# Kernel tuning notes

Hardware: AMD Instinct MI355X
Metric: run time of the kernel (lower is better)

Reference implementation:

```python
import jax, jax.numpy as jnp
import numpy as np

EPSILON = 1e-6
UP = 4
MAX_DEPTH = 10.0


def setup_inputs() -> dict:
    key = jax.random.key(0)
    k1, k2 = jax.random.split(key)
    feat = jax.random.normal(k1, (16, 4, 192, 192), dtype=jnp.float32)
    W = jax.random.normal(k2, (4, 4), dtype=jnp.float32)  # 1x1 conv weight [out,in]
    return {"feat": feat, "W": W}


def reference(feat, W):
    up = UP
    # 1x1 conv, no bias: [B,4,H,W] -> [B,4,H,W]
    plane_eq = jnp.einsum('oi,bihw->bohw', W, feat)
    # repeat_interleave upsample on H then W
    pe = jnp.repeat(jnp.repeat(plane_eq, up, axis=2), up, axis=3)
    p, q, r, s = pe[:, 0], pe[:, 1], pe[:, 2], pe[:, 3]  # [B, H*up, W*up]
    Hh, Ww = p.shape[1], p.shape[2]
    dt = feat.dtype
    base = jnp.arange(up, dtype=dt)
    # u cycles along width, v cycles along height, normalized pixel offsets
    u = (jnp.tile(base, Ww // up) - (up - 1) * 0.5) / up  # [Ww]
    v = (jnp.tile(base, Hh // up) - (up - 1) * 0.5) / up  # [Hh]
    norm = jnp.sqrt(p * p + q * q + r * r + EPSILON)
    pn = p / norm
    qn = q / norm
    rn = r / norm
    sn = s * norm
    disp = (pn * u[None, None, :] + qn * v[None, :, None] + rn) * sn
    disp = jnp.maximum(disp, 1.0 / MAX_DEPTH)[:, None]  # [B,1,Hh,Ww]
    return 1.0 / disp
```

## Files before the change

### kernel.cpp

```cpp
#include <hip/hip_runtime.h>
#include <hip/hip_bf16.h>


#define IN_H 192
#define IN_W 192
#define NBATCH 16
#define UPF 4
#define OUT_H (IN_H * UPF)
#define OUT_W (IN_W * UPF)

__global__ __launch_bounds__(256) void plane2depth_kernel(
    const float* __restrict__ feat,
    const float* __restrict__ Wm,
    float* __restrict__ out)
{
    const int npix = IN_H * IN_W;
    int idx = blockIdx.x * blockDim.x + threadIdx.x;
    if (idx >= NBATCH * npix) return;

    int b  = idx / npix;
    int hw = idx - b * npix;
    int h  = hw / IN_W;
    int w  = hw - h * IN_W;

    const float* f = feat + (size_t)b * 4 * npix + hw;
    float f0 = f[0];
    float f1 = f[npix];
    float f2 = f[2 * npix];
    float f3 = f[3 * npix];

    float p = Wm[0]  * f0 + Wm[1]  * f1 + Wm[2]  * f2 + Wm[3]  * f3;
    float q = Wm[4]  * f0 + Wm[5]  * f1 + Wm[6]  * f2 + Wm[7]  * f3;
    float r = Wm[8]  * f0 + Wm[9]  * f1 + Wm[10] * f2 + Wm[11] * f3;
    float s = Wm[12] * f0 + Wm[13] * f1 + Wm[14] * f2 + Wm[15] * f3;

    const float uv0 = -0.375f, uv1 = -0.125f, uv2 = 0.125f, uv3 = 0.375f;
    float pu0 = p * uv0, pu1 = p * uv1, pu2 = p * uv2, pu3 = p * uv3;

    float* o = out + (size_t)b * OUT_H * OUT_W + (size_t)(UPF * h) * OUT_W + UPF * w;

    const float vrow[4] = {uv0, uv1, uv2, uv3};
#pragma unroll
    for (int i = 0; i < 4; ++i) {
        float base = q * vrow[i] + r;
        float d0 = (pu0 + base) * s;
        float d1 = (pu1 + base) * s;
        float d2 = (pu2 + base) * s;
        float d3 = (pu3 + base) * s;
        float4 v4;
        v4.x = 1.0f / fmaxf(d0, 0.1f);
        v4.y = 1.0f / fmaxf(d1, 0.1f);
        v4.z = 1.0f / fmaxf(d2, 0.1f);
        v4.w = 1.0f / fmaxf(d3, 0.1f);
        *reinterpret_cast<float4*>(o + (size_t)i * OUT_W) = v4;
    }
}

extern "C" void kernel_launch(void* const* d_in, const int* in_sizes, int n_in,
                              void* d_out, int out_size, void* d_ws, size_t ws_size,
                              hipStream_t stream) {
    const float* feat = (const float*)d_in[0];
    const float* Wm   = (const float*)d_in[1];
    float* out        = (float*)d_out;

    const int total = NBATCH * IN_H * IN_W;
    const int block = 256;
    const int grid  = (total + block - 1) / block;
    plane2depth_kernel<<<grid, block, 0, stream>>>(feat, Wm, out);
}
```

Baseline: 73.04 us.

## Process two input pixels per thread with nontemporal stores and fast reciprocal

```diff
diff --git a/kernel.cpp b/kernel.cpp
--- a/kernel.cpp
+++ b/kernel.cpp
@@ -8,51 +8,67 @@
 #define UPF 4
 #define OUT_H (IN_H * UPF)
 #define OUT_W (IN_W * UPF)
+#define NPIX (IN_H * IN_W)
+#define NPAIR (NPIX / 2)
+
+typedef float f32x4 __attribute__((ext_vector_type(4)));
+typedef float f32x2 __attribute__((ext_vector_type(2)));
 
 __global__ __launch_bounds__(256) void plane2depth_kernel(
     const float* __restrict__ feat,
     const float* __restrict__ Wm,
     float* __restrict__ out)
 {
-    const int npix = IN_H * IN_W;
-    int idx = blockIdx.x * blockDim.x + threadIdx.x;
-    if (idx >= NBATCH * npix) return;
-
-    int b  = idx / npix;
-    int hw = idx - b * npix;
+    int t = blockIdx.x * blockDim.x + threadIdx.x;
+    int b  = t / NPAIR;
+    int pr = t - b * NPAIR;
+    int hw = pr * 2;
     int h  = hw / IN_W;
     int w  = hw - h * IN_W;
 
-    const float* f = feat + (size_t)b * 4 * npix + hw;
-    float f0 = f[0];
-    float f1 = f[npix];
-    float f2 = f[2 * npix];
-    float f3 = f[3 * npix];
+    const float* f = feat + (size_t)b * 4 * NPIX + hw;
+    f32x2 c0 = *reinterpret_cast<const f32x2*>(f);
+    f32x2 c1 = *reinterpret_cast<const f32x2*>(f + NPIX);
+    f32x2 c2 = *reinterpret_cast<const f32x2*>(f + 2 * NPIX);
+    f32x2 c3 = *reinterpret_cast<const f32x2*>(f + 3 * NPIX);
 
-    float p = Wm[0]  * f0 + Wm[1]  * f1 + Wm[2]  * f2 + Wm[3]  * f3;
-    float q = Wm[4]  * f0 + Wm[5]  * f1 + Wm[6]  * f2 + Wm[7]  * f3;
-    float r = Wm[8]  * f0 + Wm[9]  * f1 + Wm[10] * f2 + Wm[11] * f3;
-    float s = Wm[12] * f0 + Wm[13] * f1 + Wm[14] * f2 + Wm[15] * f3;
+    float w00 = Wm[0],  w01 = Wm[1],  w02 = Wm[2],  w03 = Wm[3];
+    float w10 = Wm[4],  w11 = Wm[5],  w12 = Wm[6],  w13 = Wm[7];
+    float w20 = Wm[8],  w21 = Wm[9],  w22 = Wm[10], w23 = Wm[11];
+    float w30 = Wm[12], w31 = Wm[13], w32 = Wm[14], w33 = Wm[15];
 
-    const float uv0 = -0.375f, uv1 = -0.125f, uv2 = 0.125f, uv3 = 0.375f;
-    float pu0 = p * uv0, pu1 = p * uv1, pu2 = p * uv2, pu3 = p * uv3;
+    float p0 = w00*c0.x + w01*c1.x + w02*c2.x + w03*c3.x;
+    float q0 = w10*c0.x + w11*c1.x + w12*c2.x + w13*c3.x;
+    float r0 = w20*c0.x + w21*c1.x + w22*c2.x + w23*c3.x;
+    float s0 = w30*c0.x + w31*c1.x + w32*c2.x + w33*c3.x;
+    float p1 = w00*c0.y + w01*c1.y + w02*c2.y + w03*c3.y;
+    float q1 = w10*c0.y + w11*c1.y + w12*c2.y + w13*c3.y;
+    float r1 = w20*c0.y + w21*c1.y + w22*c2.y + w23*c3.y;
+    float s1 = w30*c0.y + w31*c1.y + w32*c2.y + w33*c3.y;
+
+    const float uv[4] = {-0.375f, -0.125f, 0.125f, 0.375f};
+    float pu0[4], pu1[4];
+#pragma unroll
+    for (int j = 0; j < 4; ++j) { pu0[j] = p0 * uv[j]; pu1[j] = p1 * uv[j]; }
 
     float* o = out + (size_t)b * OUT_H * OUT_W + (size_t)(UPF * h) * OUT_W + UPF * w;
 
-    const float vrow[4] = {uv0, uv1, uv2, uv3};
 #pragma unroll
     for (int i = 0; i < 4; ++i) {
-        float base = q * vrow[i] + r;
-        float d0 = (pu0 + base) * s;
-        float d1 = (pu1 + base) * s;
-        float d2 = (pu2 + base) * s;
-        float d3 = (pu3 + base) * s;
-        float4 v4;
-        v4.x = 1.0f / fmaxf(d0, 0.1f);
-        v4.y = 1.0f / fmaxf(d1, 0.1f);
-        v4.z = 1.0f / fmaxf(d2, 0.1f);
-        v4.w = 1.0f / fmaxf(d3, 0.1f);
-        *reinterpret_cast<float4*>(o + (size_t)i * OUT_W) = v4;
+        float base0 = q0 * uv[i] + r0;
+        float base1 = q1 * uv[i] + r1;
+        f32x4 a, bb;
+        a.x  = __builtin_amdgcn_rcpf(fmaxf((pu0[0] + base0) * s0, 0.1f));
+        a.y  = __builtin_amdgcn_rcpf(fmaxf((pu0[1] + base0) * s0, 0.1f));
+        a.z  = __builtin_amdgcn_rcpf(fmaxf((pu0[2] + base0) * s0, 0.1f));
+        a.w  = __builtin_amdgcn_rcpf(fmaxf((pu0[3] + base0) * s0, 0.1f));
+        bb.x = __builtin_amdgcn_rcpf(fmaxf((pu1[0] + base1) * s1, 0.1f));
+        bb.y = __builtin_amdgcn_rcpf(fmaxf((pu1[1] + base1) * s1, 0.1f));
+        bb.z = __builtin_amdgcn_rcpf(fmaxf((pu1[2] + base1) * s1, 0.1f));
+        bb.w = __builtin_amdgcn_rcpf(fmaxf((pu1[3] + base1) * s1, 0.1f));
+        f32x4* row = reinterpret_cast<f32x4*>(o + (size_t)i * OUT_W);
+        __builtin_nontemporal_store(a,  row);
+        __builtin_nontemporal_store(bb, row + 1);
     }
 }
 
@@ -63,8 +79,8 @@
     const float* Wm   = (const float*)d_in[1];
     float* out        = (float*)d_out;
 
-    const int total = NBATCH * IN_H * IN_W;
+    const int total = NBATCH * NPAIR;
     const int block = 256;
-    const int grid  = (total + block - 1) / block;
+    const int grid  = total / block;
     plane2depth_kernel<<<grid, block, 0, stream>>>(feat, Wm, out);
 }
```

New measurement: 73.51 us. About the same (+0.6%).
